# Performance work log

Hardware: AMD Instinct MI355X
Metric: run time of the kernel (lower is better)

## Reference

```python
import jax, jax.numpy as jnp
import numpy as np

B, T, F = 1024, 512, 64
H1, H2, D1, D2, NOUT = 32, 16, 16, 8, 1


def setup_inputs() -> dict:
    key = jax.random.key(0)
    ks = jax.random.split(key, 14)
    s = lambda k, shape, fan: jax.random.normal(k, shape, jnp.float32) / np.sqrt(fan)
    return {
        "x": jax.random.normal(ks[0], (B, T, F), jnp.float32),
        "Wx1": s(ks[1], (F, H1), F),
        "Wh1": s(ks[2], (H1, H1), H1),
        "b1": jnp.zeros((H1,), jnp.float32),
        "Wx2": s(ks[3], (H1, H2), H1),
        "Wh2": s(ks[4], (H2, H2), H2),
        "b2": jnp.zeros((H2,), jnp.float32),
        "W3": s(ks[5], (H2, D1), H2),
        "b3": jnp.zeros((D1,), jnp.float32),
        "W4": s(ks[6], (D1, D2), D1),
        "b4": jnp.zeros((D2,), jnp.float32),
        "Wo": s(ks[7], (D2, NOUT), D2),
        "bo": jnp.zeros((NOUT,), jnp.float32),
    }


def reference(x, Wx1, Wh1, b1, Wx2, Wh2, b2, W3, b3, W4, b4, Wo, bo):
    b = x.shape[0]
    # SimpleRNN 1 (return_sequences=True): h_t = tanh(x_t Wx + h_{t-1} Wh + b)
    # Precompute input projection for all timesteps: [T, B, H1]
    xp1 = jnp.swapaxes(jnp.einsum('btf,fh->bth', x, Wx1) + b1, 0, 1)

    def step1(h, xt):
        h = jnp.tanh(xt + h @ Wh1)
        return h, h

    _, seq1 = jax.lax.scan(step1, jnp.zeros((b, Wh1.shape[0]), x.dtype), xp1)
    # SimpleRNN 2 (return_sequences=False): keep only final state
    xp2 = seq1 @ Wx2 + b2  # [T, B, H2]

    def step2(h, xt):
        h = jnp.tanh(xt + h @ Wh2)
        return h, None

    h2, _ = jax.lax.scan(step2, jnp.zeros((b, Wh2.shape[0]), x.dtype), xp2)
    # Dense head
    y = jax.nn.relu(h2 @ W3 + b3)
    y = y @ W4 + b4
    return y @ Wo + bo
```

## Files before the change

kernel.cpp:

```cpp
#include <hip/hip_runtime.h>

#define BB 1024
#define TB 512
#define FB 64
#define NH1 32
#define NH2 16
#define ND1 16
#define ND2 8

#define RD 16
#define RDM (RD - 1)
#define CHUNK 4
#define NCH (TB / CHUNK)

#define WAVE_FENCE() __builtin_amdgcn_fence(__ATOMIC_ACQ_REL, "wavefront")

__device__ __forceinline__ float tanh_fast(float v) {
    float e = __expf(2.0f * v);
    return fmaf(-2.0f, __builtin_amdgcn_rcpf(e + 1.0f), 1.0f);
}

__device__ __forceinline__ float bpermf(int byteAddr, int srcBits) {
    return __int_as_float(__builtin_amdgcn_ds_bpermute(byteAddr, srcBits));
}

__global__ __attribute__((amdgpu_flat_work_group_size(192, 192)))
           __attribute__((amdgpu_waves_per_eu(3)))
void rnn_pipe_kernel(
    const float* __restrict__ x,
    const float* __restrict__ Wx1, const float* __restrict__ Wh1, const float* __restrict__ b1,
    const float* __restrict__ Wx2, const float* __restrict__ Wh2, const float* __restrict__ b2,
    const float* __restrict__ W3,  const float* __restrict__ b3,
    const float* __restrict__ W4,  const float* __restrict__ b4,
    const float* __restrict__ Wo,  const float* __restrict__ bo,
    float* __restrict__ out)
{
    __shared__ __align__(16) float xs[4][FB];
    __shared__ __align__(16) float xpring[RD][NH1];
    __shared__ __align__(16) float h1ring[RD][NH1];
    __shared__ __align__(16) float h2s[NH2];
    __shared__ __align__(16) float ys[ND1];

    const int tid  = threadIdx.x;
    const int wid  = tid >> 6;
    const int lane = tid & 63;
    const int h = lane & 31;
    const int p = lane >> 5;
    const int g = lane & 15;
    const int q = lane >> 4;
    const int b = blockIdx.x;

    if (wid == 0) {
        auto w1 = [&](int i) { return Wx1[(32 * p + i) * NH1 + h]; };
        const float4 wxa = make_float4(w1(0),  w1(1),  w1(2),  w1(3));
        const float4 wxb = make_float4(w1(4),  w1(5),  w1(6),  w1(7));
        const float4 wxc = make_float4(w1(8),  w1(9),  w1(10), w1(11));
        const float4 wxd = make_float4(w1(12), w1(13), w1(14), w1(15));
        const float4 wxe = make_float4(w1(16), w1(17), w1(18), w1(19));
        const float4 wxf = make_float4(w1(20), w1(21), w1(22), w1(23));
        const float4 wxg = make_float4(w1(24), w1(25), w1(26), w1(27));
        const float4 wxh = make_float4(w1(28), w1(29), w1(30), w1(31));
        const float b1v = (p == 0) ? b1[h] : 0.0f;

        const float* xb = x + (size_t)b * TB * FB + lane;
        float xq0 = xb[0 * FB];
        float xq1 = xb[1 * FB];
        float xq2 = xb[2 * FB];
        float xq3 = xb[3 * FB];
        xs[0][lane] = xq0;

#define PSTEP(T, SLOT, QSTAGE, QREFILL)                                        \
    {                                                                          \
        WAVE_FENCE();                                                          \
        const int t_ = (T);                                                    \
        int tn_ = t_ + 4; tn_ = (tn_ < TB) ? tn_ : (TB - 1);                   \
        const float xnew_ = xb[(size_t)tn_ * FB];                              \
        xs[((SLOT) + 1) & 3][lane] = QSTAGE;                                   \
        const float4* xv = (const float4*)&xs[SLOT][32 * p];                   \
        float a0 = b1v, a1 = 0.0f, a2 = 0.0f, a3 = 0.0f;                       \
        float4 v_;                                                             \
        v_ = xv[0]; a0 = fmaf(v_.x, wxa.x, a0); a1 = fmaf(v_.y, wxa.y, a1);    \
                    a2 = fmaf(v_.z, wxa.z, a2); a3 = fmaf(v_.w, wxa.w, a3);    \
        v_ = xv[1]; a0 = fmaf(v_.x, wxb.x, a0); a1 = fmaf(v_.y, wxb.y, a1);    \
                    a2 = fmaf(v_.z, wxb.z, a2); a3 = fmaf(v_.w, wxb.w, a3);    \
        v_ = xv[2]; a0 = fmaf(v_.x, wxc.x, a0); a1 = fmaf(v_.y, wxc.y, a1);    \
                    a2 = fmaf(v_.z, wxc.z, a2); a3 = fmaf(v_.w, wxc.w, a3);    \
        v_ = xv[3]; a0 = fmaf(v_.x, wxd.x, a0); a1 = fmaf(v_.y, wxd.y, a1);    \
                    a2 = fmaf(v_.z, wxd.z, a2); a3 = fmaf(v_.w, wxd.w, a3);    \
        v_ = xv[4]; a0 = fmaf(v_.x, wxe.x, a0); a1 = fmaf(v_.y, wxe.y, a1);    \
                    a2 = fmaf(v_.z, wxe.z, a2); a3 = fmaf(v_.w, wxe.w, a3);    \
        v_ = xv[5]; a0 = fmaf(v_.x, wxf.x, a0); a1 = fmaf(v_.y, wxf.y, a1);    \
                    a2 = fmaf(v_.z, wxf.z, a2); a3 = fmaf(v_.w, wxf.w, a3);    \
        v_ = xv[6]; a0 = fmaf(v_.x, wxg.x, a0); a1 = fmaf(v_.y, wxg.y, a1);    \
                    a2 = fmaf(v_.z, wxg.z, a2); a3 = fmaf(v_.w, wxg.w, a3);    \
        v_ = xv[7]; a0 = fmaf(v_.x, wxh.x, a0); a1 = fmaf(v_.y, wxh.y, a1);    \
                    a2 = fmaf(v_.z, wxh.z, a2); a3 = fmaf(v_.w, wxh.w, a3);    \
        float acc = (a0 + a1) + (a2 + a3);                                     \
        acc += __shfl_xor(acc, 32, 64);                                        \
        WAVE_FENCE();                                                          \
        if (p == 0) xpring[t_ & RDM][h] = acc;                                 \
        QREFILL = xnew_;                                                       \
    }

        for (int c = 0; c < NCH + 2; ++c) {
            if (c < NCH) {
                const int t0 = c * CHUNK;
                PSTEP(t0 + 0, 0, xq1, xq0);
                PSTEP(t0 + 1, 1, xq2, xq1);
                PSTEP(t0 + 2, 2, xq3, xq2);
                PSTEP(t0 + 3, 3, xq0, xq3);
            }
            __syncthreads();
        }
#undef PSTEP

    } else if (wid == 1) {
        auto r1 = [&](int i) { return Wh1[(16 * p + i) * NH1 + h]; };
        const float4 wha = make_float4(r1(0),  r1(1),  r1(2),  r1(3));
        const float4 whb = make_float4(r1(4),  r1(5),  r1(6),  r1(7));
        const float4 whc = make_float4(r1(8),  r1(9),  r1(10), r1(11));
        const float4 whd = make_float4(r1(12), r1(13), r1(14), r1(15));
        const int bpb = 64 * p;
        float h1prev = 0.0f;

#define L1S(xpv, T)                                                            \
    {                                                                          \
        const int hh_ = __float_as_int(h1prev);                                \
        float a0 = 0.0f, a1 = 0.0f, a2 = 0.0f, a3 = 0.0f;                      \
        a0 = fmaf(bpermf(bpb +  0, hh_), wha.x, a0);                           \
        a1 = fmaf(bpermf(bpb +  4, hh_), wha.y, a1);                           \
        a2 = fmaf(bpermf(bpb +  8, hh_), wha.z, a2);                           \
        a3 = fmaf(bpermf(bpb + 12, hh_), wha.w, a3);                           \
        a0 = fmaf(bpermf(bpb + 16, hh_), whb.x, a0);                           \
        a1 = fmaf(bpermf(bpb + 20, hh_), whb.y, a1);                           \
        a2 = fmaf(bpermf(bpb + 24, hh_), whb.z, a2);                           \
        a3 = fmaf(bpermf(bpb + 28, hh_), whb.w, a3);                           \
        a0 = fmaf(bpermf(bpb + 32, hh_), whc.x, a0);                           \
        a1 = fmaf(bpermf(bpb + 36, hh_), whc.y, a1);                           \
        a2 = fmaf(bpermf(bpb + 40, hh_), whc.z, a2);                           \
        a3 = fmaf(bpermf(bpb + 44, hh_), whc.w, a3);                           \
        a0 = fmaf(bpermf(bpb + 48, hh_), whd.x, a0);                           \
        a1 = fmaf(bpermf(bpb + 52, hh_), whd.y, a1);                           \
        a2 = fmaf(bpermf(bpb + 56, hh_), whd.z, a2);                           \
        a3 = fmaf(bpermf(bpb + 60, hh_), whd.w, a3);                           \
        float acc = (a0 + a1) + (a2 + a3);                                     \
        acc += p ? 0.0f : (xpv);               \
        acc += __shfl_xor(acc, 32, 64);                                        \
        h1prev = tanh_fast(acc);                                               \
        WAVE_FENCE();                                                          \
        if (p == 0) h1ring[(T) & RDM][h] = h1prev;       \
        WAVE_FENCE();                                                          \
    }

        for (int c = 0; c < NCH + 2; ++c) {
            if (c >= 1 && c <= NCH) {
                const int t0 = (c - 1) * CHUNK;
                float xp0 = xpring[(t0 + 0) & RDM][h];
                float xp1 = xpring[(t0 + 1) & RDM][h];
                float xp2 = xpring[(t0 + 2) & RDM][h];
                float xp3 = xpring[(t0 + 3) & RDM][h];
                L1S(xp0, t0 + 0);
                L1S(xp1, t0 + 1);
                L1S(xp2, t0 + 2);
                L1S(xp3, t0 + 3);
            }
            __syncthreads();
        }
#undef L1S

    } else {
        auto w2 = [&](int i) { return Wx2[(8 * q + i) * NH2 + g]; };
        const float4 x2a = make_float4(w2(0), w2(1), w2(2), w2(3));
        const float4 x2b = make_float4(w2(4), w2(5), w2(6), w2(7));
        auto r2 = [&](int i) { return Wh2[i * NH2 + g]; };
        const float4 wh2a = make_float4(r2(0),  r2(1),  r2(2),  r2(3));
        const float4 wh2b = make_float4(r2(4),  r2(5),  r2(6),  r2(7));
        const float4 wh2c = make_float4(r2(8),  r2(9),  r2(10), r2(11));
        const float4 wh2d = make_float4(r2(12), r2(13), r2(14), r2(15));
        const float b2v = (q == 0) ? b2[g] : 0.0f;
        float h2prev = 0.0f;

#define L2S(T)                                                                 \
    {                                                                          \
        const float* hr_ = &h1ring[(T) & RDM][8 * q];                          \
        float4 u0 = *(const float4*)(hr_);                                     \
        float4 u1 = *(const float4*)(hr_ + 4);                                 \
        float cu0 = b2v, cu1 = 0.0f;                                           \
        cu0 = fmaf(u0.x, x2a.x, cu0); cu1 = fmaf(u0.y, x2a.y, cu1);            \
        cu0 = fmaf(u0.z, x2a.z, cu0); cu1 = fmaf(u0.w, x2a.w, cu1);            \
        cu0 = fmaf(u1.x, x2b.x, cu0); cu1 = fmaf(u1.y, x2b.y, cu1);            \
        cu0 = fmaf(u1.z, x2b.z, cu0); cu1 = fmaf(u1.w, x2b.w, cu1);            \
        float cu = cu0 + cu1;                                                  \
        cu += __shfl_xor(cu, 16, 64);                                          \
        cu += __shfl_xor(cu, 32, 64);                                          \
        const int h2i_ = __float_as_int(h2prev);                               \
        float c0 = 0.0f, c1 = 0.0f, c2 = 0.0f, c3 = 0.0f;                      \
        c0 = fmaf(bpermf( 0, h2i_), wh2a.x, c0);                               \
        c1 = fmaf(bpermf( 4, h2i_), wh2a.y, c1);                               \
        c2 = fmaf(bpermf( 8, h2i_), wh2a.z, c2);                               \
        c3 = fmaf(bpermf(12, h2i_), wh2a.w, c3);                               \
        c0 = fmaf(bpermf(16, h2i_), wh2b.x, c0);                               \
        c1 = fmaf(bpermf(20, h2i_), wh2b.y, c1);                               \
        c2 = fmaf(bpermf(24, h2i_), wh2b.z, c2);                               \
        c3 = fmaf(bpermf(28, h2i_), wh2b.w, c3);                               \
        c0 = fmaf(bpermf(32, h2i_), wh2c.x, c0);                               \
        c1 = fmaf(bpermf(36, h2i_), wh2c.y, c1);                               \
        c2 = fmaf(bpermf(40, h2i_), wh2c.z, c2);                               \
        c3 = fmaf(bpermf(44, h2i_), wh2c.w, c3);                               \
        c0 = fmaf(bpermf(48, h2i_), wh2d.x, c0);                               \
        c1 = fmaf(bpermf(52, h2i_), wh2d.y, c1);                               \
        c2 = fmaf(bpermf(56, h2i_), wh2d.z, c2);                               \
        c3 = fmaf(bpermf(60, h2i_), wh2d.w, c3);                               \
        float ch = (c0 + c1) + (c2 + c3);                                      \
        h2prev = tanh_fast(cu + ch);                                           \
    }

        for (int c = 0; c < NCH + 2; ++c) {
            if (c >= 2) {
                const int t0 = (c - 2) * CHUNK;
                L2S(t0 + 0);
                L2S(t0 + 1);
                L2S(t0 + 2);
                L2S(t0 + 3);
            }
            __syncthreads();
        }
#undef L2S

        WAVE_FENCE();
        if (lane < NH2) h2s[lane] = h2prev;
        WAVE_FENCE();

        float a3h = b3[g];
#pragma unroll
        for (int j = 0; j < 16; ++j) a3h = fmaf(h2s[j], W3[j * ND1 + g], a3h);
        float y1 = fmaxf(a3h, 0.0f);
        WAVE_FENCE();
        if (lane < ND1) ys[lane] = y1;
        WAVE_FENCE();

        const int e = lane & 7;
        float a4 = b4[e];
#pragma unroll
        for (int j = 0; j < 16; ++j) a4 = fmaf(ys[j], W4[j * ND2 + e], a4);

        float yo = a4 * Wo[e];
        yo += __shfl_xor(yo, 1, 64);
        yo += __shfl_xor(yo, 2, 64);
        yo += __shfl_xor(yo, 4, 64);
        if (lane == 0) out[b] = yo + bo[0];
    }
}

extern "C" void kernel_launch(void* const* d_in, const int* in_sizes, int n_in,
                              void* d_out, int out_size, void* d_ws, size_t ws_size,
                              hipStream_t stream) {
    const float* x   = (const float*)d_in[0];
    const float* Wx1 = (const float*)d_in[1];
    const float* Wh1 = (const float*)d_in[2];
    const float* b1  = (const float*)d_in[3];
    const float* Wx2 = (const float*)d_in[4];
    const float* Wh2 = (const float*)d_in[5];
    const float* b2  = (const float*)d_in[6];
    const float* W3  = (const float*)d_in[7];
    const float* b3  = (const float*)d_in[8];
    const float* W4  = (const float*)d_in[9];
    const float* b4  = (const float*)d_in[10];
    const float* Wo  = (const float*)d_in[11];
    const float* bo  = (const float*)d_in[12];
    float* out = (float*)d_out;

    rnn_pipe_kernel<<<dim3(BB), dim3(192), 0, stream>>>(
        x, Wx1, Wh1, b1, Wx2, Wh2, b2, W3, b3, W4, b4, Wo, bo, out);
}
```

Measured before the change: 355.4 us.

## Broadcast RNN hidden states through LDS instead of bpermute, double chunk size

Both recurrent layers now read the previous hidden state as float4 broadcast loads from shared-memory rings. This replaces the per-element ds_bpermute exchanges, and layer 1 computes the full 32-wide dot product per lane without a cross-half shuffle. CHUNK grows from 4 to 8, which halves the number of block-wide barriers, and the producer wave now stages and prefetches eight timesteps of x per chunk. The aim is a shorter latency of the serial recurrence per timestep, at the cost of extra LDS traffic, fences, and more registers.

```diff
diff --git a/kernel.cpp b/kernel.cpp
--- a/kernel.cpp
+++ b/kernel.cpp
@@ -10,7 +10,7 @@
 
 #define RD 16
 #define RDM (RD - 1)
-#define CHUNK 4
+#define CHUNK 8
 #define NCH (TB / CHUNK)
 
 #define WAVE_FENCE() __builtin_amdgcn_fence(__ATOMIC_ACQ_REL, "wavefront")
@@ -18,10 +18,6 @@
 __device__ __forceinline__ float tanh_fast(float v) {
     float e = __expf(2.0f * v);
     return fmaf(-2.0f, __builtin_amdgcn_rcpf(e + 1.0f), 1.0f);
-}
-
-__device__ __forceinline__ float bpermf(int byteAddr, int srcBits) {
-    return __int_as_float(__builtin_amdgcn_ds_bpermute(byteAddr, srcBits));
 }
 
 __global__ __attribute__((amdgpu_flat_work_group_size(192, 192)))
@@ -35,7 +31,7 @@
     const float* __restrict__ Wo,  const float* __restrict__ bo,
     float* __restrict__ out)
 {
-    __shared__ __align__(16) float xs[4][FB];
+    __shared__ __align__(16) float xs[CHUNK][FB];
     __shared__ __align__(16) float xpring[RD][NH1];
     __shared__ __align__(16) float h1ring[RD][NH1];
     __shared__ __align__(16) float h2s[NH2];
@@ -67,16 +63,15 @@
         float xq1 = xb[1 * FB];
         float xq2 = xb[2 * FB];
         float xq3 = xb[3 * FB];
-        xs[0][lane] = xq0;
-
-#define PSTEP(T, SLOT, QSTAGE, QREFILL)                                        \
+        float xq4 = xb[4 * FB];
+        float xq5 = xb[5 * FB];
+        float xq6 = xb[6 * FB];
+        float xq7 = xb[7 * FB];
+
+#define XPSTEP(S, T0)                                                          \
     {                                                                          \
-        WAVE_FENCE();                                                          \
-        const int t_ = (T);                                                    \
-        int tn_ = t_ + 4; tn_ = (tn_ < TB) ? tn_ : (TB - 1);                   \
-        const float xnew_ = xb[(size_t)tn_ * FB];                              \
-        xs[((SLOT) + 1) & 3][lane] = QSTAGE;                                   \
-        const float4* xv = (const float4*)&xs[SLOT][32 * p];                   \
+        const int t_ = (T0) + (S);                                             \
+        const float4* xv = (const float4*)&xs[S][32 * p];                      \
         float a0 = b1v, a1 = 0.0f, a2 = 0.0f, a3 = 0.0f;                       \
         float4 v_;                                                             \
         v_ = xv[0]; a0 = fmaf(v_.x, wxa.x, a0); a1 = fmaf(v_.y, wxa.y, a1);    \
@@ -99,138 +94,156 @@
         acc += __shfl_xor(acc, 32, 64);                                        \
         WAVE_FENCE();                                                          \
         if (p == 0) xpring[t_ & RDM][h] = acc;                                 \
-        QREFILL = xnew_;                                                       \
     }
 
         for (int c = 0; c < NCH + 2; ++c) {
             if (c < NCH) {
                 const int t0 = c * CHUNK;
-                PSTEP(t0 + 0, 0, xq1, xq0);
-                PSTEP(t0 + 1, 1, xq2, xq1);
-                PSTEP(t0 + 2, 2, xq3, xq2);
-                PSTEP(t0 + 3, 3, xq0, xq3);
+                xs[0][lane] = xq0;
+                xs[1][lane] = xq1;
+                xs[2][lane] = xq2;
+                xs[3][lane] = xq3;
+                xs[4][lane] = xq4;
+                xs[5][lane] = xq5;
+                xs[6][lane] = xq6;
+                xs[7][lane] = xq7;
+                {
+                    const int nb = (c + 1) * CHUNK;
+                    int n0 = nb + 0; n0 = (n0 < TB) ? n0 : (TB - 1);
+                    int n1 = nb + 1; n1 = (n1 < TB) ? n1 : (TB - 1);
+                    int n2 = nb + 2; n2 = (n2 < TB) ? n2 : (TB - 1);
+                    int n3 = nb + 3; n3 = (n3 < TB) ? n3 : (TB - 1);
+                    int n4 = nb + 4; n4 = (n4 < TB) ? n4 : (TB - 1);
+                    int n5 = nb + 5; n5 = (n5 < TB) ? n5 : (TB - 1);
+                    int n6 = nb + 6; n6 = (n6 < TB) ? n6 : (TB - 1);
+                    int n7 = nb + 7; n7 = (n7 < TB) ? n7 : (TB - 1);
+                    xq0 = xb[(size_t)n0 * FB];
+                    xq1 = xb[(size_t)n1 * FB];
+                    xq2 = xb[(size_t)n2 * FB];
+                    xq3 = xb[(size_t)n3 * FB];
+                    xq4 = xb[(size_t)n4 * FB];
+                    xq5 = xb[(size_t)n5 * FB];
+                    xq6 = xb[(size_t)n6 * FB];
+                    xq7 = xb[(size_t)n7 * FB];
+                }
+                XPSTEP(0, t0); XPSTEP(1, t0); XPSTEP(2, t0); XPSTEP(3, t0);
+                XPSTEP(4, t0); XPSTEP(5, t0); XPSTEP(6, t0); XPSTEP(7, t0);
             }
             __syncthreads();
         }
-#undef PSTEP
+#undef XPSTEP
 
     } else if (wid == 1) {
-        auto r1 = [&](int i) { return Wh1[(16 * p + i) * NH1 + h]; };
-        const float4 wha = make_float4(r1(0),  r1(1),  r1(2),  r1(3));
-        const float4 whb = make_float4(r1(4),  r1(5),  r1(6),  r1(7));
-        const float4 whc = make_float4(r1(8),  r1(9),  r1(10), r1(11));
-        const float4 whd = make_float4(r1(12), r1(13), r1(14), r1(15));
-        const int bpb = 64 * p;
-        float h1prev = 0.0f;
-
-#define L1S(xpv, T)                                                            \
+        auto r1f = [&](int j) { return Wh1[j * NH1 + h]; };
+        const float4 whA = make_float4(r1f(0),  r1f(1),  r1f(2),  r1f(3));
+        const float4 whB = make_float4(r1f(4),  r1f(5),  r1f(6),  r1f(7));
+        const float4 whC = make_float4(r1f(8),  r1f(9),  r1f(10), r1f(11));
+        const float4 whD = make_float4(r1f(12), r1f(13), r1f(14), r1f(15));
+        const float4 whE = make_float4(r1f(16), r1f(17), r1f(18), r1f(19));
+        const float4 whF = make_float4(r1f(20), r1f(21), r1f(22), r1f(23));
+        const float4 whG = make_float4(r1f(24), r1f(25), r1f(26), r1f(27));
+        const float4 whH = make_float4(r1f(28), r1f(29), r1f(30), r1f(31));
+
+        if (p == 0) h1ring[RDM][h] = 0.0f;
+
+#define L1S(S, T0)                                                             \
     {                                                                          \
-        const int hh_ = __float_as_int(h1prev);                                \
-        float a0 = 0.0f, a1 = 0.0f, a2 = 0.0f, a3 = 0.0f;                      \
-        a0 = fmaf(bpermf(bpb +  0, hh_), wha.x, a0);                           \
-        a1 = fmaf(bpermf(bpb +  4, hh_), wha.y, a1);                           \
-        a2 = fmaf(bpermf(bpb +  8, hh_), wha.z, a2);                           \
-        a3 = fmaf(bpermf(bpb + 12, hh_), wha.w, a3);                           \
-        a0 = fmaf(bpermf(bpb + 16, hh_), whb.x, a0);                           \
-        a1 = fmaf(bpermf(bpb + 20, hh_), whb.y, a1);                           \
-        a2 = fmaf(bpermf(bpb + 24, hh_), whb.z, a2);                           \
-        a3 = fmaf(bpermf(bpb + 28, hh_), whb.w, a3);                           \
-        a0 = fmaf(bpermf(bpb + 32, hh_), whc.x, a0);                           \
-        a1 = fmaf(bpermf(bpb + 36, hh_), whc.y, a1);                           \
-        a2 = fmaf(bpermf(bpb + 40, hh_), whc.z, a2);                           \
-        a3 = fmaf(bpermf(bpb + 44, hh_), whc.w, a3);                           \
-        a0 = fmaf(bpermf(bpb + 48, hh_), whd.x, a0);                           \
-        a1 = fmaf(bpermf(bpb + 52, hh_), whd.y, a1);                           \
-        a2 = fmaf(bpermf(bpb + 56, hh_), whd.z, a2);                           \
-        a3 = fmaf(bpermf(bpb + 60, hh_), whd.w, a3);                           \
-        float acc = (a0 + a1) + (a2 + a3);                                     \
-        acc += p ? 0.0f : (xpv);               \
-        acc += __shfl_xor(acc, 32, 64);                                        \
-        h1prev = tanh_fast(acc);                                               \
-        WAVE_FENCE();                                                          \
-        if (p == 0) h1ring[(T) & RDM][h] = h1prev;       \
+        const int t_ = (T0) + (S);                                             \
+        float xpv = xpring[t_ & RDM][h];                                       \
+        const float4* hr = (const float4*)&h1ring[(t_ - 1) & RDM][0];          \
+        float4 r0 = hr[0], r1 = hr[1], r2 = hr[2], r3 = hr[3];                 \
+        float4 r4 = hr[4], r5 = hr[5], r6 = hr[6], r7 = hr[7];                 \
+        float a0 = xpv,  a1 = 0.0f, a2 = 0.0f, a3 = 0.0f;                      \
+        float a4 = 0.0f, a5 = 0.0f, a6 = 0.0f, a7 = 0.0f;                      \
+        a0 = fmaf(r0.x, whA.x, a0); a1 = fmaf(r0.y, whA.y, a1);                \
+        a2 = fmaf(r0.z, whA.z, a2); a3 = fmaf(r0.w, whA.w, a3);                \
+        a4 = fmaf(r1.x, whB.x, a4); a5 = fmaf(r1.y, whB.y, a5);                \
+        a6 = fmaf(r1.z, whB.z, a6); a7 = fmaf(r1.w, whB.w, a7);                \
+        a0 = fmaf(r2.x, whC.x, a0); a1 = fmaf(r2.y, whC.y, a1);                \
+        a2 = fmaf(r2.z, whC.z, a2); a3 = fmaf(r2.w, whC.w, a3);                \
+        a4 = fmaf(r3.x, whD.x, a4); a5 = fmaf(r3.y, whD.y, a5);                \
+        a6 = fmaf(r3.z, whD.z, a6); a7 = fmaf(r3.w, whD.w, a7);                \
+        a0 = fmaf(r4.x, whE.x, a0); a1 = fmaf(r4.y, whE.y, a1);                \
+        a2 = fmaf(r4.z, whE.z, a2); a3 = fmaf(r4.w, whE.w, a3);                \
+        a4 = fmaf(r5.x, whF.x, a4); a5 = fmaf(r5.y, whF.y, a5);                \
+        a6 = fmaf(r5.z, whF.z, a6); a7 = fmaf(r5.w, whF.w, a7);                \
+        a0 = fmaf(r6.x, whG.x, a0); a1 = fmaf(r6.y, whG.y, a1);                \
+        a2 = fmaf(r6.z, whG.z, a2); a3 = fmaf(r6.w, whG.w, a3);                \
+        a4 = fmaf(r7.x, whH.x, a4); a5 = fmaf(r7.y, whH.y, a5);                \
+        a6 = fmaf(r7.z, whH.z, a6); a7 = fmaf(r7.w, whH.w, a7);                \
+        float acc = ((a0 + a1) + (a2 + a3)) + ((a4 + a5) + (a6 + a7));         \
+        float h1new = tanh_fast(acc);                                          \
+        WAVE_FENCE();                                                          \
+        if (p == 0) h1ring[t_ & RDM][h] = h1new;                               \
         WAVE_FENCE();                                                          \
     }
 
         for (int c = 0; c < NCH + 2; ++c) {
             if (c >= 1 && c <= NCH) {
                 const int t0 = (c - 1) * CHUNK;
-                float xp0 = xpring[(t0 + 0) & RDM][h];
-                float xp1 = xpring[(t0 + 1) & RDM][h];
-                float xp2 = xpring[(t0 + 2) & RDM][h];
-                float xp3 = xpring[(t0 + 3) & RDM][h];
-                L1S(xp0, t0 + 0);
-                L1S(xp1, t0 + 1);
-                L1S(xp2, t0 + 2);
-                L1S(xp3, t0 + 3);
+                L1S(0, t0); L1S(1, t0); L1S(2, t0); L1S(3, t0);
+                L1S(4, t0); L1S(5, t0); L1S(6, t0); L1S(7, t0);
             }
             __syncthreads();
         }
 #undef L1S
 
     } else {
-        auto w2 = [&](int i) { return Wx2[(8 * q + i) * NH2 + g]; };
-        const float4 x2a = make_float4(w2(0), w2(1), w2(2), w2(3));
-        const float4 x2b = make_float4(w2(4), w2(5), w2(6), w2(7));
-        auto r2 = [&](int i) { return Wh2[i * NH2 + g]; };
-        const float4 wh2a = make_float4(r2(0),  r2(1),  r2(2),  r2(3));
-        const float4 wh2b = make_float4(r2(4),  r2(5),  r2(6),  r2(7));
-        const float4 wh2c = make_float4(r2(8),  r2(9),  r2(10), r2(11));
-        const float4 wh2d = make_float4(r2(12), r2(13), r2(14), r2(15));
+        auto w2f = [&](int i) { return Wx2[(8 * q + i) * NH2 + g]; };
+        const float4 o2a = make_float4(w2f(0), w2f(1), w2f(2), w2f(3));
+        const float4 o2b = make_float4(w2f(4), w2f(5), w2f(6), w2f(7));
+        auto r2f = [&](int j) { return Wh2[j * NH2 + g]; };
+        const float4 w2A = make_float4(r2f(0),  r2f(1),  r2f(2),  r2f(3));
+        const float4 w2B = make_float4(r2f(4),  r2f(5),  r2f(6),  r2f(7));
+        const float4 w2C = make_float4(r2f(8),  r2f(9),  r2f(10), r2f(11));
+        const float4 w2D = make_float4(r2f(12), r2f(13), r2f(14), r2f(15));
         const float b2v = (q == 0) ? b2[g] : 0.0f;
-        float h2prev = 0.0f;
-
-#define L2S(T)                                                                 \
+
+        if (lane < NH2) h2s[lane] = 0.0f;
+
+#define L2S(S, T0)                                                             \
     {                                                                          \
-        const float* hr_ = &h1ring[(T) & RDM][8 * q];                          \
-        float4 u0 = *(const float4*)(hr_);                                     \
-        float4 u1 = *(const float4*)(hr_ + 4);                                 \
+        const int t_ = (T0) + (S);                                             \
+        const float* hrow = &h1ring[t_ & RDM][8 * q];                          \
+        float4 u0 = *(const float4*)(hrow);                                    \
+        float4 u1 = *(const float4*)(hrow + 4);                                \
+        const float4* hv = (const float4*)h2s;                                 \
+        float4 v0 = hv[0], v1 = hv[1], v2 = hv[2], v3 = hv[3];                 \
         float cu0 = b2v, cu1 = 0.0f;                                           \
-        cu0 = fmaf(u0.x, x2a.x, cu0); cu1 = fmaf(u0.y, x2a.y, cu1);            \
-        cu0 = fmaf(u0.z, x2a.z, cu0); cu1 = fmaf(u0.w, x2a.w, cu1);            \
-        cu0 = fmaf(u1.x, x2b.x, cu0); cu1 = fmaf(u1.y, x2b.y, cu1);            \
-        cu0 = fmaf(u1.z, x2b.z, cu0); cu1 = fmaf(u1.w, x2b.w, cu1);            \
+        cu0 = fmaf(u0.x, o2a.x, cu0); cu1 = fmaf(u0.y, o2a.y, cu1);            \
+        cu0 = fmaf(u0.z, o2a.z, cu0); cu1 = fmaf(u0.w, o2a.w, cu1);            \
+        cu0 = fmaf(u1.x, o2b.x, cu0); cu1 = fmaf(u1.y, o2b.y, cu1);            \
+        cu0 = fmaf(u1.z, o2b.z, cu0); cu1 = fmaf(u1.w, o2b.w, cu1);            \
         float cu = cu0 + cu1;                                                  \
         cu += __shfl_xor(cu, 16, 64);                                          \
         cu += __shfl_xor(cu, 32, 64);                                          \
-        const int h2i_ = __float_as_int(h2prev);                               \
         float c0 = 0.0f, c1 = 0.0f, c2 = 0.0f, c3 = 0.0f;                      \
-        c0 = fmaf(bpermf( 0, h2i_), wh2a.x, c0);                               \
-        c1 = fmaf(bpermf( 4, h2i_), wh2a.y, c1);                               \
-        c2 = fmaf(bpermf( 8, h2i_), wh2a.z, c2);                               \
-        c3 = fmaf(bpermf(12, h2i_), wh2a.w, c3);                               \
-        c0 = fmaf(bpermf(16, h2i_), wh2b.x, c0);                               \
-        c1 = fmaf(bpermf(20, h2i_), wh2b.y, c1);                               \
-        c2 = fmaf(bpermf(24, h2i_), wh2b.z, c2);                               \
-        c3 = fmaf(bpermf(28, h2i_), wh2b.w, c3);                               \
-        c0 = fmaf(bpermf(32, h2i_), wh2c.x, c0);                               \
-        c1 = fmaf(bpermf(36, h2i_), wh2c.y, c1);                               \
-        c2 = fmaf(bpermf(40, h2i_), wh2c.z, c2);                               \
-        c3 = fmaf(bpermf(44, h2i_), wh2c.w, c3);                               \
-        c0 = fmaf(bpermf(48, h2i_), wh2d.x, c0);                               \
-        c1 = fmaf(bpermf(52, h2i_), wh2d.y, c1);                               \
-        c2 = fmaf(bpermf(56, h2i_), wh2d.z, c2);                               \
-        c3 = fmaf(bpermf(60, h2i_), wh2d.w, c3);                               \
+        c0 = fmaf(v0.x, w2A.x, c0); c1 = fmaf(v0.y, w2A.y, c1);                \
+        c2 = fmaf(v0.z, w2A.z, c2); c3 = fmaf(v0.w, w2A.w, c3);                \
+        c0 = fmaf(v1.x, w2B.x, c0); c1 = fmaf(v1.y, w2B.y, c1);                \
+        c2 = fmaf(v1.z, w2B.z, c2); c3 = fmaf(v1.w, w2B.w, c3);                \
+        c0 = fmaf(v2.x, w2C.x, c0); c1 = fmaf(v2.y, w2C.y, c1);                \
+        c2 = fmaf(v2.z, w2C.z, c2); c3 = fmaf(v2.w, w2C.w, c3);                \
+        c0 = fmaf(v3.x, w2D.x, c0); c1 = fmaf(v3.y, w2D.y, c1);                \
+        c2 = fmaf(v3.z, w2D.z, c2); c3 = fmaf(v3.w, w2D.w, c3);                \
         float ch = (c0 + c1) + (c2 + c3);                                      \
-        h2prev = tanh_fast(cu + ch);                                           \
+        float h2new = tanh_fast(cu + ch);                                      \
+        WAVE_FENCE();                                                          \
+        if (lane < NH2) h2s[lane] = h2new;                                     \
+        WAVE_FENCE();                                                          \
     }
 
         for (int c = 0; c < NCH + 2; ++c) {
             if (c >= 2) {
                 const int t0 = (c - 2) * CHUNK;
-                L2S(t0 + 0);
-                L2S(t0 + 1);
-                L2S(t0 + 2);
-                L2S(t0 + 3);
+                L2S(0, t0); L2S(1, t0); L2S(2, t0); L2S(3, t0);
+                L2S(4, t0); L2S(5, t0); L2S(6, t0); L2S(7, t0);
             }
             __syncthreads();
         }
 #undef L2S
 
         WAVE_FENCE();
-        if (lane < NH2) h2s[lane] = h2prev;
-        WAVE_FENCE();
-
         float a3h = b3[g];
 #pragma unroll
         for (int j = 0; j < 16; ++j) a3h = fmaf(h2s[j], W3[j * ND1 + g], a3h);
```

New measurement: 335.1 us. 5.7% less time.
